# Optimization experiments

Hardware: AMD Instinct MI355X
Metric: run time of the kernel (lower is better)

The kernel has to match this reference:

```python
import jax, jax.numpy as jnp
import numpy as np

B, N, C = 8, 1024, 768
NUM_HEADS = 12
HEAD_DIM = C // NUM_HEADS  # 64
WS = 32                    # window_size[0] == window_size[1] == H == W
REL_DIM = 2 * WS - 1       # 63


def setup_inputs() -> dict:
    key = jax.random.key(0)
    ks = jax.random.split(key, 7)
    x = jax.random.normal(ks[0], (B, N, C), dtype=jnp.float32)
    qkv_w = jax.random.normal(ks[1], (3 * C, C), dtype=jnp.float32) * 0.02
    qkv_b = jnp.zeros((3 * C,), dtype=jnp.float32)
    proj_w = jax.random.normal(ks[2], (C, C), dtype=jnp.float32) * 0.02
    proj_b = jnp.zeros((C,), dtype=jnp.float32)
    rel_pos_h = jax.random.normal(ks[3], (REL_DIM, HEAD_DIM), dtype=jnp.float32) * 0.02
    rel_pos_w = jax.random.normal(ks[4], (REL_DIM, HEAD_DIM), dtype=jnp.float32) * 0.02
    return {
        "x": x,
        "qkv_w": qkv_w,
        "qkv_b": qkv_b,
        "proj_w": proj_w,
        "proj_b": proj_b,
        "rel_pos_h": rel_pos_h,
        "rel_pos_w": rel_pos_w,
        "H": WS,
        "W": WS,
    }


def reference(x, qkv_w, qkv_b, proj_w, proj_b, rel_pos_h, rel_pos_w, H, W):
    B_, N_, C_ = x.shape
    heads = NUM_HEADS
    hd = C_ // heads
    scale = hd ** -0.5

    # qkv projection: (B, N, 3, heads, hd) -> (3, B, heads, N, hd)
    qkv = (x @ qkv_w.T + qkv_b).reshape(B_, N_, 3, heads, hd).transpose(2, 0, 3, 1, 4)
    q, k, v = qkv[0], qkv[1], qkv[2]
    q = q * scale

    # raw scores (B, heads, N, N)
    attn = jnp.einsum('bhqd,bhkd->bhqk', q, k)

    # decomposed relative position bias (q_shape == k_shape -> ratios are 1.0)
    dist_h = jnp.arange(H)[:, None] - jnp.arange(H)[None, :] + (H - 1)
    dist_w = jnp.arange(W)[:, None] - jnp.arange(W)[None, :] + (W - 1)
    Rh = rel_pos_h[dist_h]  # (H, H, hd)
    Rw = rel_pos_w[dist_w]  # (W, W, hd)

    r_q = q.reshape(B_, heads, H, W, hd)
    rel_h = jnp.einsum('byhwc,hkc->byhwk', r_q, Rh)  # (B, heads, H, W, k_h)
    rel_w = jnp.einsum('byhwc,wkc->byhwk', r_q, Rw)  # (B, heads, H, W, k_w)

    attn = (attn.reshape(B_, heads, H, W, H, W)
            + rel_h[:, :, :, :, :, None]
            + rel_w[:, :, :, :, None, :]).reshape(B_, heads, N_, N_)

    attn = jax.nn.softmax(attn, axis=-1)
    out = jnp.einsum('bhqk,bhkd->bhqd', attn, v)
    out = out.transpose(0, 2, 1, 3).reshape(B_, N_, heads * hd)
    return out @ proj_w.T + proj_b
```

## Files before the change

### kernel.cpp

```cpp
#include <hip/hip_runtime.h>
#include <cstddef>

typedef short s4v __attribute__((ext_vector_type(4)));
typedef short s8v __attribute__((ext_vector_type(8)));
typedef float f4v __attribute__((ext_vector_type(4)));

__device__ __forceinline__ unsigned short f2bf(float f) {
    union { float f; unsigned u; } v; v.f = f;
    unsigned r = v.u + 0x7fff + ((v.u >> 16) & 1);
    return (unsigned short)(r >> 16);
}
__device__ __forceinline__ float bf2f(unsigned short u) {
    union { unsigned u; float f; } v; v.u = ((unsigned)u) << 16;
    return v.f;
}

__device__ __forceinline__ void gl_lds16(const void* g, void* l) {
    __builtin_amdgcn_global_load_lds(
        (const __attribute__((address_space(1))) void*)g,
        (__attribute__((address_space(3))) void*)l, 16, 0, 0);
}

#define QSC   0.18033688011112043f
#define EOFF  23.082320654223414f

__global__ __launch_bounds__(256) void to_bf16_all(
    const float* __restrict__ x, const float* __restrict__ qw,
    const float* __restrict__ pw, unsigned short* __restrict__ xd,
    unsigned short* __restrict__ qd, unsigned short* __restrict__ pd)
{
    int i = blockIdx.x * 256 + threadIdx.x;
    const float* s; unsigned short* d; int j;
    if (i < 786432)       { s = x;  d = xd; j = i; }
    else if (i < 1007616) { s = qw; d = qd; j = i - 786432; }
    else                  { s = pw; d = pd; j = i - 1007616; }
    float4 f0 = ((const float4*)s)[j * 2];
    float4 f1 = ((const float4*)s)[j * 2 + 1];
    uint4 pk;
    pk.x = (unsigned)f2bf(f0.x) | ((unsigned)f2bf(f0.y) << 16);
    pk.y = (unsigned)f2bf(f0.z) | ((unsigned)f2bf(f0.w) << 16);
    pk.z = (unsigned)f2bf(f1.x) | ((unsigned)f2bf(f1.y) << 16);
    pk.w = (unsigned)f2bf(f1.z) | ((unsigned)f2bf(f1.w) << 16);
    ((uint4*)d)[j] = pk;
}

__global__ __launch_bounds__(512) void qkv_gemm_mfma(
    const unsigned short* __restrict__ A, const unsigned short* __restrict__ W,
    const float* __restrict__ bias,
    unsigned short* __restrict__ qb, unsigned short* __restrict__ kb,
    unsigned short* __restrict__ vt)
{
    __shared__ __align__(16) unsigned short As[3][256 * 32];
    __shared__ __align__(16) unsigned short Bs[3][128 * 32];
    const int t     = threadIdx.x;
    const int lin   = blockIdx.x;
    const int xcd   = lin & 7;
    const int sq    = lin >> 3;
    const int br    = (xcd << 2) + (sq & 3);
    const int bc    = sq >> 2;
    const int wv    = t >> 6;
    const int lane  = t & 63;
    const int col16 = lane & 15;
    const int quad  = lane >> 4;
    const int w4    = lane >> 2;
    const int k8    = (lane & 3) << 3;
    const int mw    = wv >> 1;
    const int nw    = wv & 1;

    const unsigned short* Ag = A + (size_t)(br * 256 + (wv << 5) + w4) * 768 + k8;
    const unsigned short* Wg = W + (size_t)(bc * 128 + (wv << 4) + w4) * 768 + k8;
    const int woA = (wv << 5) * 32;
    const int woB = (wv << 4) * 32;

    f4v acc[4][4];
#pragma unroll
    for (int mt = 0; mt < 4; ++mt)
#pragma unroll
        for (int nt = 0; nt < 4; ++nt) {
            acc[mt][nt][0] = 0.f; acc[mt][nt][1] = 0.f;
            acc[mt][nt][2] = 0.f; acc[mt][nt][3] = 0.f;
        }

    gl_lds16(Ag,                 &As[0][woA]);
    gl_lds16(Ag + 16 * 768,      &As[0][woA + 16 * 32]);
    gl_lds16(Wg,                 &Bs[0][woB]);
    gl_lds16(Ag + 32,            &As[1][woA]);
    gl_lds16(Ag + 32 + 16 * 768, &As[1][woA + 16 * 32]);
    gl_lds16(Wg + 32,            &Bs[1][woB]);

#pragma unroll
    for (int kt = 0; kt < 24; ++kt) {
        if (kt < 22) {
            const int nb = (kt + 2) % 3;
            const int ko = (kt + 2) * 32;
            gl_lds16(Ag + ko,            &As[nb][woA]);
            gl_lds16(Ag + ko + 16 * 768, &As[nb][woA + 16 * 32]);
            gl_lds16(Wg + ko,            &Bs[nb][woB]);
        }
        if (kt < 22)       asm volatile("s_waitcnt vmcnt(6)" ::: "memory");
        else if (kt == 22) asm volatile("s_waitcnt vmcnt(3)" ::: "memory");
        else               asm volatile("s_waitcnt vmcnt(0)" ::: "memory");
        __builtin_amdgcn_s_barrier();
        asm volatile("" ::: "memory");

        const unsigned short* Ab = As[kt % 3];
        const unsigned short* Bb = Bs[kt % 3];
        s8v a[4], b[4];
#pragma unroll
        for (int mt = 0; mt < 4; ++mt)
            a[mt] = *(const s8v*)&Ab[(mw * 64 + mt * 16 + col16) * 32 + quad * 8];
#pragma unroll
        for (int nt = 0; nt < 4; ++nt)
            b[nt] = *(const s8v*)&Bb[(nw * 64 + nt * 16 + col16) * 32 + quad * 8];
#pragma unroll
        for (int mt = 0; mt < 4; ++mt)
#pragma unroll
            for (int nt = 0; nt < 4; ++nt)
                acc[mt][nt] = __builtin_amdgcn_mfma_f32_16x16x32_bf16(
                    a[mt], b[nt], acc[mt][nt], 0, 0, 0);

        asm volatile("" ::: "memory");
        __builtin_amdgcn_s_barrier();
    }

    const int which = bc / 6;
    const int cb    = (bc % 6) * 128 + nw * 64;
    const int m0    = br * 256 + mw * 64 + quad * 4;
    if (which == 2) {
#pragma unroll
        for (int nt = 0; nt < 4; ++nt) {
            int c    = cb + nt * 16 + col16;
            int head = c >> 6, d = c & 63;
            float bv = bias[1536 + c];
#pragma unroll
            for (int mt = 0; mt < 4; ++mt) {
                int mb  = m0 + mt * 16;
                int bbk = mb >> 10, tok = mb & 1023;
                uint2 pk;
                pk.x = (unsigned)f2bf(acc[mt][nt][0] + bv)
                     | ((unsigned)f2bf(acc[mt][nt][1] + bv) << 16);
                pk.y = (unsigned)f2bf(acc[mt][nt][2] + bv)
                     | ((unsigned)f2bf(acc[mt][nt][3] + bv) << 16);
                *(uint2*)&vt[((size_t)(bbk * 12 + head)) * 65536 + (size_t)d * 1024 + tok] = pk;
            }
        }
    } else {
        const float sc = (which == 0) ? QSC : 1.0f;
        unsigned short* dst = (which == 0) ? qb : kb;
#pragma unroll
        for (int nt = 0; nt < 4; ++nt) {
            int c    = cb + nt * 16 + col16;
            int head = c >> 6, d = c & 63;
            float bv = bias[which * 768 + c];
#pragma unroll
            for (int mt = 0; mt < 4; ++mt) {
#pragma unroll
                for (int i = 0; i < 4; ++i) {
                    int m   = m0 + mt * 16 + i;
                    int bbk = m >> 10, tok = m & 1023;
                    dst[(((size_t)(bbk * 12 + head) << 10) + tok) * 64 + d] =
                        f2bf((acc[mt][nt][i] + bv) * sc);
                }
            }
        }
    }
}

__global__ __launch_bounds__(512) void proj_gemm_mfma(
    const unsigned short* __restrict__ A, const unsigned short* __restrict__ W,
    const float* __restrict__ bias, float* __restrict__ Out)
{
    __shared__ __align__(16) unsigned short As[3][256 * 32];
    __shared__ __align__(16) unsigned short Bs[3][128 * 32];
    const int t     = threadIdx.x;
    const int lin   = blockIdx.x;
    const int xcd   = lin & 7;
    const int sq    = lin >> 3;
    const int br    = (xcd << 2) + (sq & 3);
    const int bc    = sq >> 2;
    const int wv    = t >> 6;
    const int lane  = t & 63;
    const int col16 = lane & 15;
    const int quad  = lane >> 4;
    const int w4    = lane >> 2;
    const int k8    = (lane & 3) << 3;
    const int mw    = wv >> 1, nw = wv & 1;

    const unsigned short* Ag = A + (size_t)(br * 256 + (wv << 5) + w4) * 768 + k8;
    const unsigned short* Wg = W + (size_t)(bc * 128 + (wv << 4) + w4) * 768 + k8;
    const int woA = (wv << 5) * 32;
    const int woB = (wv << 4) * 32;

    f4v acc[4][4];
#pragma unroll
    for (int mt = 0; mt < 4; ++mt)
#pragma unroll
        for (int nt = 0; nt < 4; ++nt) {
            acc[mt][nt][0] = 0.f; acc[mt][nt][1] = 0.f;
            acc[mt][nt][2] = 0.f; acc[mt][nt][3] = 0.f;
        }

    gl_lds16(Ag,                 &As[0][woA]);
    gl_lds16(Ag + 16 * 768,      &As[0][woA + 16 * 32]);
    gl_lds16(Wg,                 &Bs[0][woB]);
    gl_lds16(Ag + 32,            &As[1][woA]);
    gl_lds16(Ag + 32 + 16 * 768, &As[1][woA + 16 * 32]);
    gl_lds16(Wg + 32,            &Bs[1][woB]);

#pragma unroll
    for (int kt = 0; kt < 24; ++kt) {
        if (kt < 22) {
            const int nb = (kt + 2) % 3;
            const int ko = (kt + 2) * 32;
            gl_lds16(Ag + ko,            &As[nb][woA]);
            gl_lds16(Ag + ko + 16 * 768, &As[nb][woA + 16 * 32]);
            gl_lds16(Wg + ko,            &Bs[nb][woB]);
        }
        if (kt < 22)       asm volatile("s_waitcnt vmcnt(6)" ::: "memory");
        else if (kt == 22) asm volatile("s_waitcnt vmcnt(3)" ::: "memory");
        else               asm volatile("s_waitcnt vmcnt(0)" ::: "memory");
        __builtin_amdgcn_s_barrier();
        asm volatile("" ::: "memory");

        const unsigned short* Ab = As[kt % 3];
        const unsigned short* Bb = Bs[kt % 3];
        s8v a[4], b[4];
#pragma unroll
        for (int mt = 0; mt < 4; ++mt)
            a[mt] = *(const s8v*)&Ab[(mw * 64 + mt * 16 + col16) * 32 + quad * 8];
#pragma unroll
        for (int nt = 0; nt < 4; ++nt)
            b[nt] = *(const s8v*)&Bb[(nw * 64 + nt * 16 + col16) * 32 + quad * 8];
#pragma unroll
        for (int mt = 0; mt < 4; ++mt)
#pragma unroll
            for (int nt = 0; nt < 4; ++nt)
                acc[mt][nt] = __builtin_amdgcn_mfma_f32_16x16x32_bf16(
                    a[mt], b[nt], acc[mt][nt], 0, 0, 0);

        asm volatile("" ::: "memory");
        __builtin_amdgcn_s_barrier();
    }

    const int m0 = br * 256 + mw * 64 + quad * 4;
#pragma unroll
    for (int nt = 0; nt < 4; ++nt) {
        int c    = bc * 128 + nw * 64 + nt * 16 + col16;
        float bv = bias[c];
#pragma unroll
        for (int mt = 0; mt < 4; ++mt) {
#pragma unroll
            for (int i = 0; i < 4; ++i) {
                int m = m0 + mt * 16 + i;
                Out[(size_t)m * 768 + c] = acc[mt][nt][i] + bv;
            }
        }
    }
}

__global__ __launch_bounds__(256) void bias_prep_mfma(
    const unsigned short* __restrict__ Q, const float* __restrict__ Rh,
    const float* __restrict__ Rw, unsigned short* __restrict__ qhb,
    unsigned short* __restrict__ qwb)
{
    __shared__ __align__(16) char smem[36864];
    unsigned short (*Qs)[72]  = (unsigned short (*)[72])smem;
    unsigned short (*Rs)[72]  = (unsigned short (*)[72])(smem + 18432);
    unsigned short (*Wsm)[72] = (unsigned short (*)[72])(smem + 27648);
    float (*G)[66]            = (float (*)[66])smem;

    const int t    = threadIdx.x;
    const int tc8  = blockIdx.x;
    const int bh   = blockIdx.y;
    const int tok0 = tc8 << 7;

    for (int id = t; id < 1024; id += 256) {
        int row = id >> 3, g8 = (id & 7) << 3;
        *(uint4*)&Qs[row][g8] =
            *(const uint4*)(Q + ((size_t)bh * 1024 + tok0 + row) * 64 + g8);
    }
    for (int id = t; id < 512; id += 256) {
        int row = id >> 3, g8 = (id & 7) << 3;
        unsigned short* dh = &Rs[row][g8];
        unsigned short* dw = &Wsm[row][g8];
        if (row < 63) {
            const float* sh = Rh + row * 64 + g8;
            const float* sw = Rw + row * 64 + g8;
            float4 a = *(const float4*)sh; float4 b = *(const float4*)(sh + 4);
            float4 c = *(const float4*)sw; float4 d = *(const float4*)(sw + 4);
            dh[0] = f2bf(a.x); dh[1] = f2bf(a.y); dh[2] = f2bf(a.z); dh[3] = f2bf(a.w);
            dh[4] = f2bf(b.x); dh[5] = f2bf(b.y); dh[6] = f2bf(b.z); dh[7] = f2bf(b.w);
            dw[0] = f2bf(c.x); dw[1] = f2bf(c.y); dw[2] = f2bf(c.z); dw[3] = f2bf(c.w);
            dw[4] = f2bf(d.x); dw[5] = f2bf(d.y); dw[6] = f2bf(d.z); dw[7] = f2bf(d.w);
        } else {
#pragma unroll
            for (int j = 0; j < 8; ++j) { dh[j] = 0; dw[j] = 0; }
        }
    }
    __syncthreads();

    const int wv    = t >> 6;
    const int lane  = t & 63;
    const int col16 = lane & 15;
    const int quad  = lane >> 4;
    const int r0    = wv << 5;

    s8v qa[2][2], rb[4][2], wb[4][2];
#pragma unroll
    for (int mt = 0; mt < 2; ++mt)
#pragma unroll
        for (int kc = 0; kc < 2; ++kc)
            qa[mt][kc] = *(const s8v*)&Qs[r0 + mt * 16 + col16][kc * 32 + quad * 8];
#pragma unroll
    for (int nt = 0; nt < 4; ++nt)
#pragma unroll
        for (int kc = 0; kc < 2; ++kc) {
            rb[nt][kc] = *(const s8v*)&Rs[nt * 16 + col16][kc * 32 + quad * 8];
            wb[nt][kc] = *(const s8v*)&Wsm[nt * 16 + col16][kc * 32 + quad * 8];
        }

    f4v ah[2][4], aw[2][4];
#pragma unroll
    for (int mt = 0; mt < 2; ++mt)
#pragma unroll
        for (int nt = 0; nt < 4; ++nt) {
            f4v z; z[0] = 0.f; z[1] = 0.f; z[2] = 0.f; z[3] = 0.f;
            ah[mt][nt] = z; aw[mt][nt] = z;
        }
#pragma unroll
    for (int mt = 0; mt < 2; ++mt)
#pragma unroll
        for (int nt = 0; nt < 4; ++nt) {
            ah[mt][nt] = __builtin_amdgcn_mfma_f32_16x16x32_bf16(qa[mt][0], rb[nt][0], ah[mt][nt], 0, 0, 0);
            ah[mt][nt] = __builtin_amdgcn_mfma_f32_16x16x32_bf16(qa[mt][1], rb[nt][1], ah[mt][nt], 0, 0, 0);
            aw[mt][nt] = __builtin_amdgcn_mfma_f32_16x16x32_bf16(qa[mt][0], wb[nt][0], aw[mt][nt], 0, 0, 0);
            aw[mt][nt] = __builtin_amdgcn_mfma_f32_16x16x32_bf16(qa[mt][1], wb[nt][1], aw[mt][nt], 0, 0, 0);
        }
    __syncthreads();

#pragma unroll
    for (int mt = 0; mt < 2; ++mt)
#pragma unroll
        for (int nt = 0; nt < 4; ++nt)
#pragma unroll
            for (int i = 0; i < 4; ++i)
                G[r0 + mt * 16 + quad * 4 + i][nt * 16 + col16] = ah[mt][nt][i];
    __syncthreads();
    for (int id = t; id < 2048; id += 256) {
        int tok = id >> 4, c2 = (id & 15) << 1;
        int i_img = (tc8 << 2) + (tok >> 5);
        float g0 = G[tok][i_img - c2 + 31];
        float g1 = G[tok][i_img - c2 + 30];
        unsigned pk = (unsigned)f2bf(g0) | ((unsigned)f2bf(g1) << 16);
        *(unsigned*)&qhb[(((size_t)bh << 10) + tok0 + tok) * 32 + c2] = pk;
    }
    __syncthreads();

#pragma unroll
    for (int mt = 0; mt < 2; ++mt)
#pragma unroll
        for (int nt = 0; nt < 4; ++nt)
#pragma unroll
            for (int i = 0; i < 4; ++i)
                G[r0 + mt * 16 + quad * 4 + i][nt * 16 + col16] = aw[mt][nt][i];
    __syncthreads();
    for (int id = t; id < 2048; id += 256) {
        int tok = id >> 4, c2 = (id & 15) << 1;
        int j = tok & 31;
        float g0 = G[tok][j - c2 + 31];
        float g1 = G[tok][j - c2 + 30];
        unsigned pk = (unsigned)f2bf(g0) | ((unsigned)f2bf(g1) << 16);
        *(unsigned*)&qwb[(((size_t)bh << 10) + tok0 + tok) * 32 + c2] = pk;
    }
}

__global__ __launch_bounds__(256, 6) void attn_mfma(
    const unsigned short* __restrict__ Q, const unsigned short* __restrict__ K,
    const unsigned short* __restrict__ Vt,
    const unsigned short* __restrict__ qhb, const unsigned short* __restrict__ qwb,
    unsigned short* __restrict__ Out)
{
    const int t  = threadIdx.x;
    const int id  = blockIdx.x;
    const int xcd = id & 7;
    const int wq  = id >> 3;
    const int bh  = xcd * 12 + (wq % 12);
    const int qt2 = wq / 12;
    const int b   = bh / 12;
    const int h   = bh - b * 12;
    const int q0  = qt2 << 6;

    __shared__ __align__(16) unsigned short Ks[64 * 64];
    __shared__ __align__(16) unsigned short Vs[64 * 64];
    __shared__ float qh_s[64][33];

    const unsigned short* Kp = K  + (size_t)bh * 65536;
    const unsigned short* Vp = Vt + (size_t)bh * 65536;

    {
        const unsigned* qhp = (const unsigned*)(qhb + ((size_t)bh * 1024 + q0) * 32);
        for (int i2 = t; i2 < 1024; i2 += 256) {
            int row = i2 >> 4, c2 = (i2 & 15) << 1;
            unsigned ph = qhp[i2];
            qh_s[row][c2]     = bf2f((unsigned short)(ph & 0xffff)) - EOFF;
            qh_s[row][c2 + 1] = bf2f((unsigned short)(ph >> 16))    - EOFF;
        }
    }

    const int wv = t >> 6;
    const int lane = t & 63;
    const int c  = lane & 15;
    const int qd = lane >> 4;

    s8v qf0, qf1;
    float uw[8];
    {
        const size_t row = (size_t)bh * 1024 + q0 + (wv << 4) + c;
        const unsigned short* qp = Q + row * 64 + qd * 8;
        qf0 = *(const s8v*)qp;
        qf1 = *(const s8v*)(qp + 32);
        s8v w8 = *(const s8v*)(qwb + row * 32 + qd * 8);
#pragma unroll
        for (int j = 0; j < 8; ++j) uw[j] = bf2f((unsigned short)w8[j]);
    }

    const int xlo = (qd     ^ (c & 7)) << 3;
    const int xhi = ((qd+4) ^ (c & 7)) << 3;

    const int e0 = t * 8, e1 = t * 8 + 2048;
    const int g0 = e0 >> 6, g1 = e1 >> 6;
    const int c8 = t & 7;
    const int s0 = c8 << 3, s1 = s0;
    const int L0 = (g0 & 32) | ((g0 & 4) << 2) | ((g0 & 24) >> 1) | (g0 & 3);
    const int L1 = (g1 & 32) | ((g1 & 4) << 2) | ((g1 & 24) >> 1) | (g1 & 3);
    const int kw0 = L0 * 64 + ((c8 ^ (L0 & 7)) << 3);
    const int kw1 = L1 * 64 + ((c8 ^ (L1 & 7)) << 3);
    const int vw0 = g0 * 64 + ((c8 ^ (g0 & 7)) << 3);
    const int vw1 = g1 * 64 + ((c8 ^ (g1 & 7)) << 3);
    {
        uint4 pk0 = *(const uint4*)(Kp + e0);
        uint4 pk1 = *(const uint4*)(Kp + e1);
        uint4 pv0 = *(const uint4*)(Vp + (size_t)g0 * 1024 + s0);
        uint4 pv1 = *(const uint4*)(Vp + (size_t)g1 * 1024 + s1);
        *(uint4*)&Ks[kw0] = pk0;
        *(uint4*)&Ks[kw1] = pk1;
        *(uint4*)&Vs[vw0] = pv0;
        *(uint4*)&Vs[vw1] = pv1;
    }
    __syncthreads();

    f4v o[4];
#pragma unroll
    for (int dt = 0; dt < 4; ++dt) { o[dt][0] = 0.f; o[dt][1] = 0.f; o[dt][2] = 0.f; o[dt][3] = 0.f; }
    float lp = 0.f;

    for (int kt = 0; kt < 16; ++kt) {
        uint4 pk0, pk1, pv0, pv1;
        if (kt < 15) {
            const int k0n = (kt + 1) << 6;
            pk0 = *(const uint4*)(Kp + (size_t)k0n * 64 + e0);
            pk1 = *(const uint4*)(Kp + (size_t)k0n * 64 + e1);
            pv0 = *(const uint4*)(Vp + (size_t)g0 * 1024 + k0n + s0);
            pv1 = *(const uint4*)(Vp + (size_t)g1 * 1024 + k0n + s1);
        }

        f4v sc[4];
#pragma unroll
        for (int T = 0; T < 4; ++T) {
            s8v lo = *(const s8v*)&Ks[(T * 16 + c) * 64 + xlo];
            s8v hi = *(const s8v*)&Ks[(T * 16 + c) * 64 + xhi];
            f4v z; z[0] = 0.f; z[1] = 0.f; z[2] = 0.f; z[3] = 0.f;
            z = __builtin_amdgcn_mfma_f32_16x16x32_bf16(lo, qf0, z, 0, 0, 0);
            z = __builtin_amdgcn_mfma_f32_16x16x32_bf16(hi, qf1, z, 0, 0, 0);
            sc[T] = z;
        }

        const float qhv0 = qh_s[(wv << 4) + c][(kt << 1)];
        const float qhv1 = qh_s[(wv << 4) + c][(kt << 1) + 1];

        s8v pa0, pa1;
#pragma unroll
        for (int j = 0; j < 4; ++j) {
            float pe = __builtin_amdgcn_exp2f(sc[0][j] + qhv0 + uw[j]);
            lp += pe; pa0[j] = (short)f2bf(pe);
        }
#pragma unroll
        for (int j = 0; j < 4; ++j) {
            float pe = __builtin_amdgcn_exp2f(sc[1][j] + qhv0 + uw[4 + j]);
            lp += pe; pa0[4 + j] = (short)f2bf(pe);
        }
#pragma unroll
        for (int j = 0; j < 4; ++j) {
            float pe = __builtin_amdgcn_exp2f(sc[2][j] + qhv1 + uw[j]);
            lp += pe; pa1[j] = (short)f2bf(pe);
        }
#pragma unroll
        for (int j = 0; j < 4; ++j) {
            float pe = __builtin_amdgcn_exp2f(sc[3][j] + qhv1 + uw[4 + j]);
            lp += pe; pa1[4 + j] = (short)f2bf(pe);
        }

#pragma unroll
        for (int dt = 0; dt < 4; ++dt) {
            s8v vlo = *(const s8v*)&Vs[(dt * 16 + c) * 64 + xlo];
            s8v vhi = *(const s8v*)&Vs[(dt * 16 + c) * 64 + xhi];
            o[dt] = __builtin_amdgcn_mfma_f32_16x16x32_bf16(pa0, vlo, o[dt], 0, 0, 0);
            o[dt] = __builtin_amdgcn_mfma_f32_16x16x32_bf16(pa1, vhi, o[dt], 0, 0, 0);
        }

        __syncthreads();
        if (kt < 15) {
            *(uint4*)&Ks[kw0] = pk0;
            *(uint4*)&Ks[kw1] = pk1;
            *(uint4*)&Vs[vw0] = pv0;
            *(uint4*)&Vs[vw1] = pv1;
        }
        __syncthreads();
    }

    lp += __shfl_xor(lp, 16);
    lp += __shfl_xor(lp, 32);

#pragma unroll
    for (int i = 0; i < 4; ++i) {
        float inv = 1.f / __shfl(lp, (qd << 2) + i);
        int qr = q0 + (wv << 4) + (qd << 2) + i;
        unsigned short* dst = Out + ((size_t)b * 1024 + qr) * 768 + h * 64;
#pragma unroll
        for (int dt = 0; dt < 4; ++dt)
            dst[dt * 16 + c] = f2bf(o[dt][i] * inv);
    }
}

extern "C" void kernel_launch(void* const* d_in, const int* in_sizes, int n_in,
                              void* d_out, int out_size, void* d_ws, size_t ws_size,
                              hipStream_t stream) {
    const float* x      = (const float*)d_in[0];
    const float* qkv_w  = (const float*)d_in[1];
    const float* qkv_b  = (const float*)d_in[2];
    const float* proj_w = (const float*)d_in[3];
    const float* proj_b = (const float*)d_in[4];
    const float* rel_h  = (const float*)d_in[5];
    const float* rel_w  = (const float*)d_in[6];
    float* out = (float*)d_out;

    char* ws = (char*)d_ws;
    unsigned short* qbuf  = (unsigned short*)(ws);
    unsigned short* kbuf  = (unsigned short*)(ws + 12582912);
    unsigned short* vtbuf = (unsigned short*)(ws + 25165824);
    unsigned short* xab   = (unsigned short*)(ws + 37748736);
    unsigned short* wqb   = (unsigned short*)(ws + 50331648);
    unsigned short* wpb   = (unsigned short*)(ws + 53870592);
    unsigned short* qhb   = (unsigned short*)(ws + 55050240);
    unsigned short* qwb   = (unsigned short*)(ws + 61341696);

    to_bf16_all<<<4224, 256, 0, stream>>>(x, qkv_w, proj_w, xab, wqb, wpb);
    qkv_gemm_mfma<<<576, 512, 0, stream>>>(xab, wqb, qkv_b, qbuf, kbuf, vtbuf);
    bias_prep_mfma<<<dim3(8, 96), 256, 0, stream>>>(qbuf, rel_h, rel_w, qhb, qwb);
    attn_mfma<<<1536, 256, 0, stream>>>(qbuf, kbuf, vtbuf, qhb, qwb, xab);
    proj_gemm_mfma<<<192, 512, 0, stream>>>(xab, wpb, proj_b, out);
}
```

Measured before the change: 210.4 us.

## Process 128 queries per attention block so each K/V tile serves two query groups

Each attention block now covers 128 query rows instead of 64, with each wave computing two 16-row query groups against the same K/V fragments held in LDS and registers. This halves the number of blocks and the K/V global loads and LDS fills per query, and reuses each K fragment read across two MFMA chains. In exchange it doubles accumulator and Q registers per thread, lowers the occupancy hint from 6 to 3 blocks, and leaves fewer blocks (768) to fill the GPU.

Result: no change. 206.6 us (-1.8%).

```diff
diff --git a/kernel.cpp b/kernel.cpp
--- a/kernel.cpp
+++ b/kernel.cpp
@@ -374,7 +374,7 @@
     }
 }
 
-__global__ __launch_bounds__(256, 6) void attn_mfma(
+__global__ __launch_bounds__(256, 3) void attn_mfma(
     const unsigned short* __restrict__ Q, const unsigned short* __restrict__ K,
     const unsigned short* __restrict__ Vt,
     const unsigned short* __restrict__ qhb, const unsigned short* __restrict__ qwb,
@@ -385,21 +385,21 @@
     const int xcd = id & 7;
     const int wq  = id >> 3;
     const int bh  = xcd * 12 + (wq % 12);
-    const int qt2 = wq / 12;
+    const int qt  = wq / 12;
     const int b   = bh / 12;
     const int h   = bh - b * 12;
-    const int q0  = qt2 << 6;
+    const int q0  = qt << 7;
 
     __shared__ __align__(16) unsigned short Ks[64 * 64];
     __shared__ __align__(16) unsigned short Vs[64 * 64];
-    __shared__ float qh_s[64][33];
+    __shared__ float qh_s[128][33];
 
     const unsigned short* Kp = K  + (size_t)bh * 65536;
     const unsigned short* Vp = Vt + (size_t)bh * 65536;
 
     {
         const unsigned* qhp = (const unsigned*)(qhb + ((size_t)bh * 1024 + q0) * 32);
-        for (int i2 = t; i2 < 1024; i2 += 256) {
+        for (int i2 = t; i2 < 2048; i2 += 256) {
             int row = i2 >> 4, c2 = (i2 & 15) << 1;
             unsigned ph = qhp[i2];
             qh_s[row][c2]     = bf2f((unsigned short)(ph & 0xffff)) - EOFF;
@@ -412,16 +412,22 @@
     const int c  = lane & 15;
     const int qd = lane >> 4;
 
-    s8v qf0, qf1;
-    float uw[8];
+    s8v qfA0, qfA1, qfB0, qfB1;
+    float uwA[8], uwB[8];
     {
-        const size_t row = (size_t)bh * 1024 + q0 + (wv << 4) + c;
-        const unsigned short* qp = Q + row * 64 + qd * 8;
-        qf0 = *(const s8v*)qp;
-        qf1 = *(const s8v*)(qp + 32);
-        s8v w8 = *(const s8v*)(qwb + row * 32 + qd * 8);
-#pragma unroll
-        for (int j = 0; j < 8; ++j) uw[j] = bf2f((unsigned short)w8[j]);
+        const size_t rowA = (size_t)bh * 1024 + q0 + (wv << 5) + c;
+        const unsigned short* qpA = Q + rowA * 64 + qd * 8;
+        qfA0 = *(const s8v*)qpA;
+        qfA1 = *(const s8v*)(qpA + 32);
+        s8v w8A = *(const s8v*)(qwb + rowA * 32 + qd * 8);
+        const size_t rowB = rowA + 16;
+        const unsigned short* qpB = Q + rowB * 64 + qd * 8;
+        qfB0 = *(const s8v*)qpB;
+        qfB1 = *(const s8v*)(qpB + 32);
+        s8v w8B = *(const s8v*)(qwb + rowB * 32 + qd * 8);
+#pragma unroll
+        for (int j = 0; j < 8; ++j) { uwA[j] = bf2f((unsigned short)w8A[j]);
+                                      uwB[j] = bf2f((unsigned short)w8B[j]); }
     }
 
     const int xlo = (qd     ^ (c & 7)) << 3;
@@ -430,7 +436,7 @@
     const int e0 = t * 8, e1 = t * 8 + 2048;
     const int g0 = e0 >> 6, g1 = e1 >> 6;
     const int c8 = t & 7;
-    const int s0 = c8 << 3, s1 = s0;
+    const int s0 = c8 << 3;
     const int L0 = (g0 & 32) | ((g0 & 4) << 2) | ((g0 & 24) >> 1) | (g0 & 3);
     const int L1 = (g1 & 32) | ((g1 & 4) << 2) | ((g1 & 24) >> 1) | (g1 & 3);
     const int kw0 = L0 * 64 + ((c8 ^ (L0 & 7)) << 3);
@@ -441,7 +447,7 @@
         uint4 pk0 = *(const uint4*)(Kp + e0);
         uint4 pk1 = *(const uint4*)(Kp + e1);
         uint4 pv0 = *(const uint4*)(Vp + (size_t)g0 * 1024 + s0);
-        uint4 pv1 = *(const uint4*)(Vp + (size_t)g1 * 1024 + s1);
+        uint4 pv1 = *(const uint4*)(Vp + (size_t)g1 * 1024 + s0);
         *(uint4*)&Ks[kw0] = pk0;
         *(uint4*)&Ks[kw1] = pk1;
         *(uint4*)&Vs[vw0] = pv0;
@@ -449,10 +455,15 @@
     }
     __syncthreads();
 
-    f4v o[4];
-#pragma unroll
-    for (int dt = 0; dt < 4; ++dt) { o[dt][0] = 0.f; o[dt][1] = 0.f; o[dt][2] = 0.f; o[dt][3] = 0.f; }
-    float lp = 0.f;
+    f4v o[2][4];
+#pragma unroll
+    for (int qg = 0; qg < 2; ++qg)
+#pragma unroll
+        for (int dt = 0; dt < 4; ++dt) {
+            o[qg][dt][0] = 0.f; o[qg][dt][1] = 0.f;
+            o[qg][dt][2] = 0.f; o[qg][dt][3] = 0.f;
+        }
+    float lp[2] = {0.f, 0.f};
 
     for (int kt = 0; kt < 16; ++kt) {
         uint4 pk0, pk1, pv0, pv1;
@@ -461,51 +472,67 @@
             pk0 = *(const uint4*)(Kp + (size_t)k0n * 64 + e0);
             pk1 = *(const uint4*)(Kp + (size_t)k0n * 64 + e1);
             pv0 = *(const uint4*)(Vp + (size_t)g0 * 1024 + k0n + s0);
-            pv1 = *(const uint4*)(Vp + (size_t)g1 * 1024 + k0n + s1);
-        }
-
-        f4v sc[4];
+            pv1 = *(const uint4*)(Vp + (size_t)g1 * 1024 + k0n + s0);
+        }
+
+        s8v klo[4], khi[4];
 #pragma unroll
         for (int T = 0; T < 4; ++T) {
-            s8v lo = *(const s8v*)&Ks[(T * 16 + c) * 64 + xlo];
-            s8v hi = *(const s8v*)&Ks[(T * 16 + c) * 64 + xhi];
-            f4v z; z[0] = 0.f; z[1] = 0.f; z[2] = 0.f; z[3] = 0.f;
-            z = __builtin_amdgcn_mfma_f32_16x16x32_bf16(lo, qf0, z, 0, 0, 0);
-            z = __builtin_amdgcn_mfma_f32_16x16x32_bf16(hi, qf1, z, 0, 0, 0);
-            sc[T] = z;
-        }
-
-        const float qhv0 = qh_s[(wv << 4) + c][(kt << 1)];
-        const float qhv1 = qh_s[(wv << 4) + c][(kt << 1) + 1];
-
-        s8v pa0, pa1;
-#pragma unroll
-        for (int j = 0; j < 4; ++j) {
-            float pe = __builtin_amdgcn_exp2f(sc[0][j] + qhv0 + uw[j]);
-            lp += pe; pa0[j] = (short)f2bf(pe);
-        }
-#pragma unroll
-        for (int j = 0; j < 4; ++j) {
-            float pe = __builtin_amdgcn_exp2f(sc[1][j] + qhv0 + uw[4 + j]);
-            lp += pe; pa0[4 + j] = (short)f2bf(pe);
-        }
-#pragma unroll
-        for (int j = 0; j < 4; ++j) {
-            float pe = __builtin_amdgcn_exp2f(sc[2][j] + qhv1 + uw[j]);
-            lp += pe; pa1[j] = (short)f2bf(pe);
-        }
-#pragma unroll
-        for (int j = 0; j < 4; ++j) {
-            float pe = __builtin_amdgcn_exp2f(sc[3][j] + qhv1 + uw[4 + j]);
-            lp += pe; pa1[4 + j] = (short)f2bf(pe);
+            klo[T] = *(const s8v*)&Ks[(T * 16 + c) * 64 + xlo];
+            khi[T] = *(const s8v*)&Ks[(T * 16 + c) * 64 + xhi];
+        }
+
+        s8v pa[2][2];
+#pragma unroll
+        for (int qg = 0; qg < 2; ++qg) {
+            const s8v qf0 = qg ? qfB0 : qfA0;
+            const s8v qf1 = qg ? qfB1 : qfA1;
+            const float* uw = qg ? uwB : uwA;
+            const int qrow = (wv << 5) + qg * 16 + c;
+
+            f4v sc[4];
+#pragma unroll
+            for (int T = 0; T < 4; ++T) {
+                f4v z; z[0] = 0.f; z[1] = 0.f; z[2] = 0.f; z[3] = 0.f;
+                z = __builtin_amdgcn_mfma_f32_16x16x32_bf16(klo[T], qf0, z, 0, 0, 0);
+                z = __builtin_amdgcn_mfma_f32_16x16x32_bf16(khi[T], qf1, z, 0, 0, 0);
+                sc[T] = z;
+            }
+
+            const float qhv0 = qh_s[qrow][(kt << 1)];
+            const float qhv1 = qh_s[qrow][(kt << 1) + 1];
+
+#pragma unroll
+            for (int j = 0; j < 4; ++j) {
+                float pe = __builtin_amdgcn_exp2f(sc[0][j] + qhv0 + uw[j]);
+                lp[qg] += pe; pa[qg][0][j] = (short)f2bf(pe);
+            }
+#pragma unroll
+            for (int j = 0; j < 4; ++j) {
+                float pe = __builtin_amdgcn_exp2f(sc[1][j] + qhv0 + uw[4 + j]);
+                lp[qg] += pe; pa[qg][0][4 + j] = (short)f2bf(pe);
+            }
+#pragma unroll
+            for (int j = 0; j < 4; ++j) {
+                float pe = __builtin_amdgcn_exp2f(sc[2][j] + qhv1 + uw[j]);
+                lp[qg] += pe; pa[qg][1][j] = (short)f2bf(pe);
+            }
+#pragma unroll
+            for (int j = 0; j < 4; ++j) {
+                float pe = __builtin_amdgcn_exp2f(sc[3][j] + qhv1 + uw[4 + j]);
+                lp[qg] += pe; pa[qg][1][4 + j] = (short)f2bf(pe);
+            }
         }
 
 #pragma unroll
         for (int dt = 0; dt < 4; ++dt) {
             s8v vlo = *(const s8v*)&Vs[(dt * 16 + c) * 64 + xlo];
             s8v vhi = *(const s8v*)&Vs[(dt * 16 + c) * 64 + xhi];
-            o[dt] = __builtin_amdgcn_mfma_f32_16x16x32_bf16(pa0, vlo, o[dt], 0, 0, 0);
-            o[dt] = __builtin_amdgcn_mfma_f32_16x16x32_bf16(pa1, vhi, o[dt], 0, 0, 0);
+#pragma unroll
+            for (int qg = 0; qg < 2; ++qg) {
+                o[qg][dt] = __builtin_amdgcn_mfma_f32_16x16x32_bf16(pa[qg][0], vlo, o[qg][dt], 0, 0, 0);
+                o[qg][dt] = __builtin_amdgcn_mfma_f32_16x16x32_bf16(pa[qg][1], vhi, o[qg][dt], 0, 0, 0);
+            }
         }
 
         __syncthreads();
@@ -518,17 +545,19 @@
         __syncthreads();
     }
 
-    lp += __shfl_xor(lp, 16);
-    lp += __shfl_xor(lp, 32);
-
-#pragma unroll
-    for (int i = 0; i < 4; ++i) {
-        float inv = 1.f / __shfl(lp, (qd << 2) + i);
-        int qr = q0 + (wv << 4) + (qd << 2) + i;
-        unsigned short* dst = Out + ((size_t)b * 1024 + qr) * 768 + h * 64;
-#pragma unroll
-        for (int dt = 0; dt < 4; ++dt)
-            dst[dt * 16 + c] = f2bf(o[dt][i] * inv);
+#pragma unroll
+    for (int qg = 0; qg < 2; ++qg) {
+        lp[qg] += __shfl_xor(lp[qg], 16);
+        lp[qg] += __shfl_xor(lp[qg], 32);
+#pragma unroll
+        for (int i = 0; i < 4; ++i) {
+            float inv = 1.f / __shfl(lp[qg], (qd << 2) + i);
+            int qr = q0 + (wv << 5) + qg * 16 + (qd << 2) + i;
+            unsigned short* dst = Out + ((size_t)b * 1024 + qr) * 768 + h * 64;
+#pragma unroll
+            for (int dt = 0; dt < 4; ++dt)
+                dst[dt * 16 + c] = f2bf(o[qg][dt][i] * inv);
+        }
     }
 }
 
@@ -557,6 +586,6 @@
     to_bf16_all<<<4224, 256, 0, stream>>>(x, qkv_w, proj_w, xab, wqb, wpb);
     qkv_gemm_mfma<<<576, 512, 0, stream>>>(xab, wqb, qkv_b, qbuf, kbuf, vtbuf);
     bias_prep_mfma<<<dim3(8, 96), 256, 0, stream>>>(qbuf, rel_h, rel_w, qhb, qwb);
-    attn_mfma<<<1536, 256, 0, stream>>>(qbuf, kbuf, vtbuf, qhb, qwb, xab);
+    attn_mfma<<<768, 256, 0, stream>>>(qbuf, kbuf, vtbuf, qhb, qwb, xab);
     proj_gemm_mfma<<<192, 512, 0, stream>>>(xab, wpb, proj_b, out);
 }
```
